# Performance work log

Measured on AMD Instinct MI355X. Metric: run time of the kernel, lower is better.

The kernel has to match this reference:

```python
import jax, jax.numpy as jnp
import numpy as np

N_NODES = 25000
N_EDGES = 400000
FEAT = 128
HID = 64
HEADS = 4
NUM_CLASSES = 2
NUM_GRAPHS = 64


def setup_inputs() -> dict:
    key = jax.random.key(0)
    ks = jax.random.split(key, 16)
    x = jax.random.normal(ks[0], (N_NODES, FEAT), dtype=jnp.float32)
    edge_index = jax.random.randint(ks[1], (2, N_EDGES), 0, N_NODES, dtype=jnp.int32)
    batch = jnp.sort(jax.random.randint(ks[2], (N_NODES,), 0, NUM_GRAPHS, dtype=jnp.int32))
    s = 1.0 / np.sqrt(FEAT)
    sh = 1.0 / np.sqrt(HID)
    shc = 1.0 / np.sqrt(HID * HEADS)
    return {
        "x": x,
        "edge_index": edge_index,
        "batch": batch,
        # conv1: GraphConv(FEAT -> HID): lin_rel (bias) on aggregated neighbors + lin_root (no bias)
        "W1_rel": jax.random.uniform(ks[3], (FEAT, HID), jnp.float32, -s, s),
        "b1": jnp.zeros((HID,), jnp.float32),
        "W1_root": jax.random.uniform(ks[4], (FEAT, HID), jnp.float32, -s, s),
        # conv3: GATConv(HID -> HID, heads=HEADS), concat output [N, HEADS*HID]
        "Wg": jax.random.uniform(ks[5], (HID, HEADS * HID), jnp.float32, -sh, sh),
        "att_src": jax.random.uniform(ks[6], (HEADS, HID), jnp.float32, -sh, sh),
        "att_dst": jax.random.uniform(ks[7], (HEADS, HID), jnp.float32, -sh, sh),
        "bg": jnp.zeros((HEADS * HID,), jnp.float32),
        # conv5: GraphConv(HEADS*HID -> HID)
        "W5_rel": jax.random.uniform(ks[8], (HEADS * HID, HID), jnp.float32, -shc, shc),
        "b5": jnp.zeros((HID,), jnp.float32),
        "W5_root": jax.random.uniform(ks[9], (HEADS * HID, HID), jnp.float32, -shc, shc),
        # fc head
        "W_fc1": jax.random.uniform(ks[10], (HID, HID), jnp.float32, -sh, sh),
        "b_fc1": jnp.zeros((HID,), jnp.float32),
        "W_fc2": jax.random.uniform(ks[11], (HID, NUM_CLASSES), jnp.float32, -sh, sh),
        "b_fc2": jnp.zeros((NUM_CLASSES,), jnp.float32),
    }


def _graph_conv(h, src, dst, W_rel, b, W_root):
    # PyG GraphConv (aggr='add'): out_i = W_rel @ sum_{j->i} h_j + b + W_root @ h_i
    agg = jax.ops.segment_sum(h[src], dst, num_segments=N_NODES)
    return agg @ W_rel + b + h @ W_root


def _gat_conv(h, src, dst, Wg, att_src, att_dst, bg):
    # GATConv with default add_self_loops=True; eval mode (no attn dropout)
    n = h.shape[0]
    loop = jnp.arange(n, dtype=src.dtype)
    si = jnp.concatenate([src, loop])
    di = jnp.concatenate([dst, loop])
    xl = (h @ Wg).reshape(n, HEADS, HID)              # [N, H, C]
    a_s = jnp.sum(xl * att_src, axis=-1)              # [N, H]
    a_d = jnp.sum(xl * att_dst, axis=-1)              # [N, H]
    e = jax.nn.leaky_relu(a_s[si] + a_d[di], 0.2)     # [E', H]
    m = jax.ops.segment_max(e, di, num_segments=n)
    p = jnp.exp(e - m[di])
    denom = jax.ops.segment_sum(p, di, num_segments=n)
    alpha = p / denom[di]                             # segment softmax over incoming edges
    out = jax.ops.segment_sum(alpha[:, :, None] * xl[si], di, num_segments=n)
    return out.reshape(n, HEADS * HID) + bg


def reference(x, edge_index, batch, W1_rel, b1, W1_root, Wg, att_src, att_dst, bg,
              W5_rel, b5, W5_root, W_fc1, b_fc1, W_fc2, b_fc2):
    src, dst = edge_index[0], edge_index[1]
    h = jax.nn.relu(_graph_conv(x, src, dst, W1_rel, b1, W1_root))
    h = jax.nn.relu(_gat_conv(h, src, dst, Wg, att_src, att_dst, bg))
    h = jax.nn.relu(_graph_conv(h, src, dst, W5_rel, b5, W5_root))
    g = jax.ops.segment_sum(h, batch, num_segments=NUM_GRAPHS)   # global_add_pool
    g = jax.nn.relu(g @ W_fc1 + b_fc1)
    return jax.nn.sigmoid(g @ W_fc2 + b_fc2)
```

## Files before the change

### kernel.cpp

```cpp
#include <hip/hip_runtime.h>
#include <math.h>

#define N_NODES 25000
#define N_EDGES 400000
#define FEAT 128
#define HID 64
#define HEADS 4
#define HH 256
#define NUM_GRAPHS 64
#define BUCKET 96

typedef unsigned short ushort_t;
typedef unsigned int uint_t;
typedef __attribute__((ext_vector_type(8))) short short8;
typedef __attribute__((ext_vector_type(4))) float f32x4;

__device__ __forceinline__ float lrelu(float x){ return x > 0.f ? x : 0.2f*x; }

__device__ __forceinline__ ushort_t f2bf(float f){
  uint_t u = __float_as_uint(f);
  return (ushort_t)((u + 0x7fffu + ((u >> 16) & 1u)) >> 16);
}
#define BF_LO(u) __uint_as_float((u) << 16)
#define BF_HI(u) __uint_as_float((u) & 0xffff0000u)

__global__ __launch_bounds__(256) void k_pack(
    const float* __restrict__ W1_rel, const float* __restrict__ W1_root,
    const float* __restrict__ W5_rel, const float* __restrict__ W5_root,
    const float* __restrict__ Wg,
    ushort_t* __restrict__ wc1b, ushort_t* __restrict__ wc5b,
    ushort_t* __restrict__ wgb)
{
  const int e = blockIdx.x*256 + threadIdx.x;
  {
    int j=e&7, lane=(e>>3)&63, kc=(e>>9)&3, nt=e>>11;
    int k = kc*32 + (lane>>4)*8 + j, n = nt*16 + (lane&15);
    float v = (n < 64) ? W1_rel[k*64 + n] : W1_root[k*64 + n - 64];
    wc1b[e] = f2bf(v);
  }
  {
    int j=e&7, lane=(e>>3)&63, kt=(e>>9)&1, nt=e>>10;
    int k = kt*32 + (lane>>4)*8 + j, n = nt*16 + (lane&15);
    wgb[e] = f2bf(Wg[k*HH + n]);
  }
  #pragma unroll
  for (int e5 = e; e5 < 32768; e5 += 16384){
    int j=e5&7, lane=(e5>>3)&63, kc=(e5>>9)&7, nt=e5>>12;
    int k = kc*32 + (lane>>4)*8 + j, n = nt*16 + (lane&15);
    float v = (n < 64) ? W5_rel[k*64 + n] : W5_root[k*64 + n - 64];
    wc5b[e5] = f2bf(v);
  }
}

__global__ __launch_bounds__(256) void conv1_mfma(
    const float* __restrict__ X, const ushort_t* __restrict__ wc1b,
    const float* __restrict__ bias,
    ushort_t* __restrict__ out_rel_b, float* __restrict__ out_root)
{
  const int wid  = __builtin_amdgcn_readfirstlane(threadIdx.x >> 6);
  const int lane = threadIdx.x & 63;
  const int quad = lane >> 4, col = lane & 15;
  const int nb = blockIdx.x*64 + wid*16;
  if (nb >= N_NODES) return;
  const int row = min(nb + col, N_NODES-1);
  const float* __restrict__ xr = X + (size_t)row*FEAT + quad*8;
  short8 a[4];
  #pragma unroll
  for (int kc = 0; kc < 4; kc++){
    #pragma unroll
    for (int j = 0; j < 8; j++)
      ((ushort_t*)&a[kc])[j] = f2bf(xr[kc*32 + j]);
  }
  #pragma unroll
  for (int nt = 0; nt < 8; nt++){
    f32x4 d = {0.f,0.f,0.f,0.f};
    #pragma unroll
    for (int kc = 0; kc < 4; kc++){
      short8 b = *(const short8*)(wc1b + ((size_t)(nt*4+kc)*64 + lane)*8);
      d = __builtin_amdgcn_mfma_f32_16x16x32_bf16(a[kc], b, d, 0, 0, 0);
    }
    if (nt < 4){
      #pragma unroll
      for (int r = 0; r < 4; r++){
        const int node = nb + quad*4 + r;
        if (node < N_NODES)
          out_rel_b[(size_t)node*HID + nt*16 + col] = f2bf(d[r]);
      }
    } else {
      const float bv = bias[(nt-4)*16 + col];
      #pragma unroll
      for (int r = 0; r < 4; r++){
        const int node = nb + quad*4 + r;
        if (node < N_NODES)
          out_root[(size_t)node*HID + (nt-4)*16 + col] = d[r] + bv;
      }
    }
  }
}

__global__ __launch_bounds__(256) void conv5_mfma(
    const ushort_t* __restrict__ h2b, const ushort_t* __restrict__ wc5b,
    const float* __restrict__ bias,
    ushort_t* __restrict__ out_rel_b, float* __restrict__ out_root)
{
  const int wid  = __builtin_amdgcn_readfirstlane(threadIdx.x >> 6);
  const int lane = threadIdx.x & 63;
  const int quad = lane >> 4, col = lane & 15;
  const int nb = blockIdx.x*64 + wid*16;
  if (nb >= N_NODES) return;
  const ushort_t* __restrict__ arow = h2b + (size_t)(nb + col)*HH + quad*8;
  short8 a[8];
  #pragma unroll
  for (int kc = 0; kc < 8; kc++)
    a[kc] = *(const short8*)(arow + kc*32);
  #pragma unroll
  for (int nt = 0; nt < 8; nt++){
    f32x4 d = {0.f,0.f,0.f,0.f};
    #pragma unroll
    for (int kc = 0; kc < 8; kc++){
      short8 b = *(const short8*)(wc5b + ((size_t)(nt*8+kc)*64 + lane)*8);
      d = __builtin_amdgcn_mfma_f32_16x16x32_bf16(a[kc], b, d, 0, 0, 0);
    }
    if (nt < 4){
      #pragma unroll
      for (int r = 0; r < 4; r++){
        const int node = nb + quad*4 + r;
        if (node < N_NODES)
          out_rel_b[(size_t)node*HID + nt*16 + col] = f2bf(d[r]);
      }
    } else {
      const float bv = bias[(nt-4)*16 + col];
      #pragma unroll
      for (int r = 0; r < 4; r++){
        const int node = nb + quad*4 + r;
        if (node < N_NODES)
          out_root[(size_t)node*HID + (nt-4)*16 + col] = d[r] + bv;
      }
    }
  }
}

__global__ __launch_bounds__(256) void k3_mfma(
    const ushort_t* __restrict__ h1b, const ushort_t* __restrict__ wgb,
    const float* __restrict__ att_src, const float* __restrict__ att_dst,
    ushort_t* __restrict__ xlb, float* __restrict__ a_s, float* __restrict__ a_d)
{
  const int wid  = __builtin_amdgcn_readfirstlane(threadIdx.x >> 6);
  const int lane = threadIdx.x & 63;
  const int quad = lane >> 4, col = lane & 15;
  const int nb = blockIdx.x*64 + wid*16;
  const ushort_t* arow = h1b + (size_t)(nb + col)*HID + quad*8;
  short8 a0 = *(const short8*)(arow);
  short8 a1 = *(const short8*)(arow + 32);
  float as_acc[4] = {0,0,0,0}, ad_acc[4] = {0,0,0,0};
  #pragma unroll
  for (int nt = 0; nt < 16; nt++){
    short8 b0 = *(const short8*)(wgb + ((size_t)(nt*2+0)*64 + lane)*8);
    short8 b1 = *(const short8*)(wgb + ((size_t)(nt*2+1)*64 + lane)*8);
    f32x4 d = {0.f, 0.f, 0.f, 0.f};
    d = __builtin_amdgcn_mfma_f32_16x16x32_bf16(a0, b0, d, 0, 0, 0);
    d = __builtin_amdgcn_mfma_f32_16x16x32_bf16(a1, b1, d, 0, 0, 0);
    const int h = nt >> 2;
    const float asv = att_src[h*HID + (nt & 3)*16 + col];
    const float adv = att_dst[h*HID + (nt & 3)*16 + col];
    #pragma unroll
    for (int r = 0; r < 4; r++){
      const int node = nb + quad*4 + r;
      if (node < N_NODES)
        xlb[(size_t)node*HH + nt*16 + col] = f2bf(d[r]);
      as_acc[r] += d[r]*asv;
      ad_acc[r] += d[r]*adv;
    }
    if ((nt & 3) == 3){
      #pragma unroll
      for (int r = 0; r < 4; r++){
        float s1 = as_acc[r], s2 = ad_acc[r];
        #pragma unroll
        for (int off = 1; off < 16; off <<= 1){
          s1 += __shfl_xor(s1, off, 64);
          s2 += __shfl_xor(s2, off, 64);
        }
        const int node = nb + quad*4 + r;
        if (col == 0 && node < N_NODES){
          a_s[node*HEADS + h] = s1;
          a_d[node*HEADS + h] = s2;
        }
        as_acc[r] = 0.f; ad_acc[r] = 0.f;
      }
    }
  }
}

__global__ __launch_bounds__(256) void k_fill(const int* __restrict__ src,
                                              const int* __restrict__ dst,
                                              int* __restrict__ cnt,
                                              int* __restrict__ slot)
{
  int e = blockIdx.x*256 + threadIdx.x;
  if (e >= N_EDGES) return;
  int d = dst[e];
  int pos = atomicAdd(&cnt[d], 1);
  if (pos < BUCKET) slot[(size_t)d*BUCKET + pos] = src[e];
}

template<bool BF16OUT>
__global__ __launch_bounds__(256) void k_aggb(
    const int* __restrict__ cnt, const int* __restrict__ slot,
    const ushort_t* __restrict__ featb, const float* __restrict__ root,
    float* __restrict__ outf, ushort_t* __restrict__ outb)
{
  const int node = blockIdx.x*4 + (threadIdx.x >> 6);
  const int lane = threadIdx.x & 63;
  const int* __restrict__ sl = slot + (size_t)node*BUCKET;
  const int deg = min(cnt[node], BUCKET);
  float acc = root[(size_t)node*HID + lane];
  int e = 0;
  for (; e + 4 <= deg; e += 4){
    int sA = sl[e],   sB = sl[e+1];
    int sC = sl[e+2], sD = sl[e+3];
    float xA = BF_LO((uint_t)featb[(size_t)sA*HID + lane]);
    float xB = BF_LO((uint_t)featb[(size_t)sB*HID + lane]);
    float xC = BF_LO((uint_t)featb[(size_t)sC*HID + lane]);
    float xD = BF_LO((uint_t)featb[(size_t)sD*HID + lane]);
    acc += xA; acc += xB; acc += xC; acc += xD;
  }
  for (; e < deg; e++){
    int s = sl[e];
    acc += BF_LO((uint_t)featb[(size_t)s*HID + lane]);
  }
  const float v = fmaxf(acc, 0.f);
  if (BF16OUT) outb[(size_t)node*HID + lane] = f2bf(v);
  else         outf[(size_t)node*HID + lane] = v;
}

__global__ __launch_bounds__(256) void k_gat_node(
    const int* __restrict__ cnt, const int* __restrict__ slot,
    const uint2* __restrict__ xl2,
    const float* __restrict__ a_s, const float* __restrict__ a_d,
    const float* __restrict__ bg, ushort_t* __restrict__ h2b)
{
  const int node = blockIdx.x*4 + (threadIdx.x >> 6);
  const int lane = threadIdx.x & 63;
  const int h  = lane >> 4;
  const int el = lane & 15;
  const int* __restrict__ sl = slot + (size_t)node*BUCKET;
  const int deg = min(cnt[node], BUCKET);
  const float adh = a_d[node*HEADS + h];
  float acc0=0, acc1=0, acc2=0, acc3=0;
  float dsum = 0.f;
  for (int base = 0; base < deg; base += 16){
    float pme = 0.f; int sme = node;
    const int e = base + el;
    if (e < deg){
      sme = sl[e];
      pme = __expf(lrelu(a_s[sme*HEADS + h] + adh));
    }
    dsum += pme;
    const int nsub = min(16, deg - base);
    int e4 = 0;
    for (; e4 + 2 <= nsub; e4 += 2){
      const int b0 = (lane & 48) + e4;
      const float pA = __shfl(pme, b0, 64);
      const int   sA = __shfl(sme, b0, 64);
      const float pB = __shfl(pme, b0 + 1, 64);
      const int   sB = __shfl(sme, b0 + 1, 64);
      uint2 rA = xl2[(size_t)sA*64 + lane];
      uint2 rB = xl2[(size_t)sB*64 + lane];
      acc0 += pA*BF_LO(rA.x); acc1 += pA*BF_HI(rA.x);
      acc2 += pA*BF_LO(rA.y); acc3 += pA*BF_HI(rA.y);
      acc0 += pB*BF_LO(rB.x); acc1 += pB*BF_HI(rB.x);
      acc2 += pB*BF_LO(rB.y); acc3 += pB*BF_HI(rB.y);
    }
    if (e4 < nsub){
      const int b0 = (lane & 48) + e4;
      const float pA = __shfl(pme, b0, 64);
      const int   sA = __shfl(sme, b0, 64);
      uint2 rA = xl2[(size_t)sA*64 + lane];
      acc0 += pA*BF_LO(rA.x); acc1 += pA*BF_HI(rA.x);
      acc2 += pA*BF_LO(rA.y); acc3 += pA*BF_HI(rA.y);
    }
  }
  #pragma unroll
  for (int off = 1; off < 16; off <<= 1) dsum += __shfl_xor(dsum, off, 64);
  const float pself = __expf(lrelu(a_s[node*HEADS + h] + adh));
  const float inv = 1.f / (dsum + pself);
  uint2 r = xl2[(size_t)node*64 + lane];
  acc0 += pself*BF_LO(r.x); acc1 += pself*BF_HI(r.x);
  acc2 += pself*BF_LO(r.y); acc3 += pself*BF_HI(r.y);
  const int col0 = lane*4;
  const float ox = fmaxf(acc0*inv + bg[col0+0], 0.f);
  const float oy = fmaxf(acc1*inv + bg[col0+1], 0.f);
  const float oz = fmaxf(acc2*inv + bg[col0+2], 0.f);
  const float ow = fmaxf(acc3*inv + bg[col0+3], 0.f);
  uint2 o;
  o.x = (uint_t)f2bf(ox) | ((uint_t)f2bf(oy) << 16);
  o.y = (uint_t)f2bf(oz) | ((uint_t)f2bf(ow) << 16);
  ((uint2*)(h2b + (size_t)node*HH))[lane] = o;
}

__global__ __launch_bounds__(256) void k_pool(
    const float* __restrict__ h3, const int* __restrict__ batch,
    float* __restrict__ g)
{
  const int w = blockIdx.x*4 + (threadIdx.x >> 6);
  const int j = threadIdx.x & 63;
  int n0 = w*64;
  if (n0 >= N_NODES) return;
  int n1 = min(n0+64, N_NODES);
  float acc = 0.f;
  int cur = batch[n0];
  for (int n = n0; n < n1; n++){
    int b = batch[n];
    if (b != cur){ atomicAdd(&g[cur*HID + j], acc); acc = 0.f; cur = b; }
    acc += h3[n*HID + j];
  }
  atomicAdd(&g[cur*HID + j], acc);
}

__global__ __launch_bounds__(256) void k_head(
    const float* __restrict__ g, const float* __restrict__ W1,
    const float* __restrict__ b1, const float* __restrict__ W2,
    const float* __restrict__ b2, float* __restrict__ out)
{
  __shared__ float gs[NUM_GRAPHS*HID];
  __shared__ float hh[NUM_GRAPHS*HID];
  for (int i = threadIdx.x; i < NUM_GRAPHS*HID; i += 256) gs[i] = g[i];
  __syncthreads();
  for (int t = threadIdx.x; t < NUM_GRAPHS*HID; t += 256){
    int b = t >> 6, j = t & 63;
    float acc = b1[j];
    for (int k = 0; k < HID; k++) acc += gs[b*HID+k]*W1[k*HID+j];
    hh[t] = fmaxf(acc, 0.f);
  }
  __syncthreads();
  for (int t = threadIdx.x; t < NUM_GRAPHS*2; t += 256){
    int b = t >> 1, c = t & 1;
    float acc = b2[c];
    for (int k = 0; k < HID; k++) acc += hh[b*HID+k]*W2[k*2+c];
    out[t] = 1.f / (1.f + __expf(-acc));
  }
}

extern "C" void kernel_launch(void* const* d_in, const int* in_sizes, int n_in,
                              void* d_out, int out_size, void* d_ws, size_t ws_size,
                              hipStream_t stream)
{
  const float* x       = (const float*)d_in[0];
  const int*   ei      = (const int*)d_in[1];
  const int*   batch   = (const int*)d_in[2];
  const float* W1_rel  = (const float*)d_in[3];
  const float* b1      = (const float*)d_in[4];
  const float* W1_root = (const float*)d_in[5];
  const float* Wg      = (const float*)d_in[6];
  const float* att_src = (const float*)d_in[7];
  const float* att_dst = (const float*)d_in[8];
  const float* bg      = (const float*)d_in[9];
  const float* W5_rel  = (const float*)d_in[10];
  const float* b5      = (const float*)d_in[11];
  const float* W5_root = (const float*)d_in[12];
  const float* W_fc1   = (const float*)d_in[13];
  const float* b_fc1   = (const float*)d_in[14];
  const float* W_fc2   = (const float*)d_in[15];
  const float* b_fc2   = (const float*)d_in[16];
  const int* src = ei;
  const int* dst = ei + N_EDGES;

  float* ws    = (float*)d_ws;
  ushort_t* xr_b = (ushort_t*)ws;
  float* hB    = ws +   800000;
  ushort_t* h1b = (ushort_t*)(ws + 2400000);
  ushort_t* xlb = (ushort_t*)(ws + 3200768);
  float* a_s   = ws +  6400768;
  float* a_d   = ws +  6500768;
  ushort_t* h2b = (ushort_t*)(ws + 6600768);
  float* g     = ws +  9803840;
  int*   cnt   = (int*)(ws + 9807936);
  ushort_t* wc1b = (ushort_t*)(ws + 9833600);
  ushort_t* wc5b = (ushort_t*)(ws + 9841792);
  ushort_t* wgb  = (ushort_t*)(ws + 9858176);
  int*   slot  = (int*)(ws + 9870000);
  float* out   = (float*)d_out;

  hipMemsetAsync(g, 0, (4096 + N_NODES)*sizeof(float), stream);
  k_fill<<<(N_EDGES+255)/256,256,0,stream>>>(src, dst, cnt, slot);
  k_pack<<<64,256,0,stream>>>(W1_rel, W1_root, W5_rel, W5_root, Wg,
                              wc1b, wc5b, wgb);

  conv1_mfma<<<(N_NODES+63)/64,256,0,stream>>>(x, wc1b, b1, xr_b, hB);
  k_aggb<true><<<N_NODES/4,256,0,stream>>>(cnt, slot, xr_b, hB, nullptr, h1b);

  k3_mfma<<<(N_NODES+63)/64,256,0,stream>>>(h1b, wgb, att_src, att_dst,
                                            xlb, a_s, a_d);
  k_gat_node<<<N_NODES/4,256,0,stream>>>(cnt, slot,
      (const uint2*)xlb, a_s, a_d, bg, h2b);

  conv5_mfma<<<(N_NODES+63)/64,256,0,stream>>>(h2b, wc5b, b5, xr_b, hB);
  k_aggb<false><<<N_NODES/4,256,0,stream>>>(cnt, slot, xr_b, hB, hB, nullptr);

  k_pool<<<(N_NODES/256)+1,256,0,stream>>>(hB, batch, g);
  k_head<<<1,256,0,stream>>>(g, W_fc1, b_fc1, W_fc2, b_fc2, out);
}
```

Measured before the change: 255.1 us.

## Split GAT features into head-major planes and parallelize GAT aggregation per head

Stores the GAT projected features, attention scores and GAT output in head-major planes, so each head's 64-wide slice is a contiguous 128-byte row. The GAT aggregation kernel now runs one block per (node group, head), with four edges gathered concurrently per wave and a cross-group shuffle reduction at the end. conv5 reads its input from the head-major planes. The weight-packing kernel is also folded into the edge-bucketing kernel to save a launch. This raises gather parallelism and spreads head work across four times as many blocks, at the cost of redundant neighbor-index and degree reads per head, extra shuffles, and a guard that skips zero-probability lanes.

```diff
diff --git a/kernel.cpp b/kernel.cpp
--- a/kernel.cpp
+++ b/kernel.cpp
@@ -9,6 +9,8 @@
 #define HH 256
 #define NUM_GRAPHS 64
 #define BUCKET 96
+#define HS 1601536
+#define NPH 25600
 
 typedef unsigned short ushort_t;
 typedef unsigned int uint_t;
@@ -24,7 +26,9 @@
 #define BF_LO(u) __uint_as_float((u) << 16)
 #define BF_HI(u) __uint_as_float((u) & 0xffff0000u)
 
-__global__ __launch_bounds__(256) void k_pack(
+__global__ __launch_bounds__(256) void k_fill(
+    const int* __restrict__ src, const int* __restrict__ dst,
+    int* __restrict__ cnt, int* __restrict__ slot,
     const float* __restrict__ W1_rel, const float* __restrict__ W1_root,
     const float* __restrict__ W5_rel, const float* __restrict__ W5_root,
     const float* __restrict__ Wg,
@@ -32,23 +36,30 @@
     ushort_t* __restrict__ wgb)
 {
   const int e = blockIdx.x*256 + threadIdx.x;
-  {
-    int j=e&7, lane=(e>>3)&63, kc=(e>>9)&3, nt=e>>11;
-    int k = kc*32 + (lane>>4)*8 + j, n = nt*16 + (lane&15);
-    float v = (n < 64) ? W1_rel[k*64 + n] : W1_root[k*64 + n - 64];
-    wc1b[e] = f2bf(v);
-  }
-  {
-    int j=e&7, lane=(e>>3)&63, kt=(e>>9)&1, nt=e>>10;
-    int k = kt*32 + (lane>>4)*8 + j, n = nt*16 + (lane&15);
-    wgb[e] = f2bf(Wg[k*HH + n]);
-  }
-  #pragma unroll
-  for (int e5 = e; e5 < 32768; e5 += 16384){
-    int j=e5&7, lane=(e5>>3)&63, kc=(e5>>9)&7, nt=e5>>12;
-    int k = kc*32 + (lane>>4)*8 + j, n = nt*16 + (lane&15);
-    float v = (n < 64) ? W5_rel[k*64 + n] : W5_root[k*64 + n - 64];
-    wc5b[e5] = f2bf(v);
+  if (blockIdx.x < 64){
+    {
+      int j=e&7, lane=(e>>3)&63, kc=(e>>9)&3, nt=e>>11;
+      int k = kc*32 + (lane>>4)*8 + j, n = nt*16 + (lane&15);
+      float v = (n < 64) ? W1_rel[k*64 + n] : W1_root[k*64 + n - 64];
+      wc1b[e] = f2bf(v);
+    }
+    {
+      int j=e&7, lane=(e>>3)&63, kt=(e>>9)&1, nt=e>>10;
+      int k = kt*32 + (lane>>4)*8 + j, n = nt*16 + (lane&15);
+      wgb[e] = f2bf(Wg[k*HH + n]);
+    }
+    #pragma unroll
+    for (int e5 = e; e5 < 32768; e5 += 16384){
+      int j=e5&7, lane=(e5>>3)&63, kc=(e5>>9)&7, nt=e5>>12;
+      int k = kc*32 + (lane>>4)*8 + j, n = nt*16 + (lane&15);
+      float v = (n < 64) ? W5_rel[k*64 + n] : W5_root[k*64 + n - 64];
+      wc5b[e5] = f2bf(v);
+    }
+  }
+  if (e < N_EDGES){
+    int d = dst[e];
+    int pos = atomicAdd(&cnt[d], 1);
+    if (pos < BUCKET) slot[(size_t)d*BUCKET + pos] = src[e];
   }
 }
 
@@ -99,7 +110,7 @@
 }
 
 __global__ __launch_bounds__(256) void conv5_mfma(
-    const ushort_t* __restrict__ h2b, const ushort_t* __restrict__ wc5b,
+    const ushort_t* __restrict__ h2b_hm, const ushort_t* __restrict__ wc5b,
     const float* __restrict__ bias,
     ushort_t* __restrict__ out_rel_b, float* __restrict__ out_root)
 {
@@ -108,11 +119,14 @@
   const int quad = lane >> 4, col = lane & 15;
   const int nb = blockIdx.x*64 + wid*16;
   if (nb >= N_NODES) return;
-  const ushort_t* __restrict__ arow = h2b + (size_t)(nb + col)*HH + quad*8;
+  const int row = nb + col;
   short8 a[8];
   #pragma unroll
-  for (int kc = 0; kc < 8; kc++)
-    a[kc] = *(const short8*)(arow + kc*32);
+  for (int kc = 0; kc < 8; kc++){
+    const int k0 = kc*32 + quad*8;
+    a[kc] = *(const short8*)(h2b_hm + (size_t)(k0>>6)*HS
+                             + (size_t)row*HID + (k0&63));
+  }
   #pragma unroll
   for (int nt = 0; nt < 8; nt++){
     f32x4 d = {0.f,0.f,0.f,0.f};
@@ -143,7 +157,8 @@
 __global__ __launch_bounds__(256) void k3_mfma(
     const ushort_t* __restrict__ h1b, const ushort_t* __restrict__ wgb,
     const float* __restrict__ att_src, const float* __restrict__ att_dst,
-    ushort_t* __restrict__ xlb, float* __restrict__ a_s, float* __restrict__ a_d)
+    ushort_t* __restrict__ xlb_hm, float* __restrict__ a_s_hm,
+    float* __restrict__ a_d_hm)
 {
   const int wid  = __builtin_amdgcn_readfirstlane(threadIdx.x >> 6);
   const int lane = threadIdx.x & 63;
@@ -167,7 +182,7 @@
     for (int r = 0; r < 4; r++){
       const int node = nb + quad*4 + r;
       if (node < N_NODES)
-        xlb[(size_t)node*HH + nt*16 + col] = f2bf(d[r]);
+        xlb_hm[(size_t)h*HS + (size_t)node*HID + (nt&3)*16 + col] = f2bf(d[r]);
       as_acc[r] += d[r]*asv;
       ad_acc[r] += d[r]*adv;
     }
@@ -182,25 +197,13 @@
         }
         const int node = nb + quad*4 + r;
         if (col == 0 && node < N_NODES){
-          a_s[node*HEADS + h] = s1;
-          a_d[node*HEADS + h] = s2;
+          a_s_hm[h*NPH + node] = s1;
+          a_d_hm[h*NPH + node] = s2;
         }
         as_acc[r] = 0.f; ad_acc[r] = 0.f;
       }
     }
   }
-}
-
-__global__ __launch_bounds__(256) void k_fill(const int* __restrict__ src,
-                                              const int* __restrict__ dst,
-                                              int* __restrict__ cnt,
-                                              int* __restrict__ slot)
-{
-  int e = blockIdx.x*256 + threadIdx.x;
-  if (e >= N_EDGES) return;
-  int d = dst[e];
-  int pos = atomicAdd(&cnt[d], 1);
-  if (pos < BUCKET) slot[(size_t)d*BUCKET + pos] = src[e];
 }
 
 template<bool BF16OUT>
@@ -235,67 +238,63 @@
 
 __global__ __launch_bounds__(256) void k_gat_node(
     const int* __restrict__ cnt, const int* __restrict__ slot,
-    const uint2* __restrict__ xl2,
-    const float* __restrict__ a_s, const float* __restrict__ a_d,
-    const float* __restrict__ bg, ushort_t* __restrict__ h2b)
-{
-  const int node = blockIdx.x*4 + (threadIdx.x >> 6);
+    const ushort_t* __restrict__ xlb_hm, const float* __restrict__ a_s_hm,
+    const float* __restrict__ a_d_hm, const float* __restrict__ bg,
+    ushort_t* __restrict__ h2b_hm)
+{
+  const int head = blockIdx.x & 3;
+  const int node = (blockIdx.x >> 2)*4 + (threadIdx.x >> 6);
   const int lane = threadIdx.x & 63;
-  const int h  = lane >> 4;
-  const int el = lane & 15;
+  const int eg = lane >> 4, cl = lane & 15;
   const int* __restrict__ sl = slot + (size_t)node*BUCKET;
   const int deg = min(cnt[node], BUCKET);
-  const float adh = a_d[node*HEADS + h];
+  const ushort_t* __restrict__ xlh = xlb_hm + (size_t)head*HS;
+  const float* __restrict__ ash = a_s_hm + head*NPH;
+  const float adh = a_d_hm[head*NPH + node];
   float acc0=0, acc1=0, acc2=0, acc3=0;
   float dsum = 0.f;
   for (int base = 0; base < deg; base += 16){
     float pme = 0.f; int sme = node;
-    const int e = base + el;
+    const int e = base + cl;
     if (e < deg){
       sme = sl[e];
-      pme = __expf(lrelu(a_s[sme*HEADS + h] + adh));
-    }
-    dsum += pme;
-    const int nsub = min(16, deg - base);
-    int e4 = 0;
-    for (; e4 + 2 <= nsub; e4 += 2){
-      const int b0 = (lane & 48) + e4;
-      const float pA = __shfl(pme, b0, 64);
-      const int   sA = __shfl(sme, b0, 64);
-      const float pB = __shfl(pme, b0 + 1, 64);
-      const int   sB = __shfl(sme, b0 + 1, 64);
-      uint2 rA = xl2[(size_t)sA*64 + lane];
-      uint2 rB = xl2[(size_t)sB*64 + lane];
-      acc0 += pA*BF_LO(rA.x); acc1 += pA*BF_HI(rA.x);
-      acc2 += pA*BF_LO(rA.y); acc3 += pA*BF_HI(rA.y);
-      acc0 += pB*BF_LO(rB.x); acc1 += pB*BF_HI(rB.x);
-      acc2 += pB*BF_LO(rB.y); acc3 += pB*BF_HI(rB.y);
-    }
-    if (e4 < nsub){
-      const int b0 = (lane & 48) + e4;
-      const float pA = __shfl(pme, b0, 64);
-      const int   sA = __shfl(sme, b0, 64);
-      uint2 rA = xl2[(size_t)sA*64 + lane];
-      acc0 += pA*BF_LO(rA.x); acc1 += pA*BF_HI(rA.x);
-      acc2 += pA*BF_LO(rA.y); acc3 += pA*BF_HI(rA.y);
-    }
-  }
+      pme = __expf(lrelu(ash[sme] + adh));
+    }
+    if (eg == 0) dsum += pme;
+    #pragma unroll
+    for (int s = 0; s < 4; s++){
+      const int e2 = s*4 + eg;
+      const float p = __shfl(pme, e2, 64);
+      if (p > 0.f){
+        const int sidx = __shfl(sme, e2, 64);
+        uint2 r = ((const uint2*)(xlh + (size_t)sidx*HID))[cl];
+        acc0 += p*BF_LO(r.x); acc1 += p*BF_HI(r.x);
+        acc2 += p*BF_LO(r.y); acc3 += p*BF_HI(r.y);
+      }
+    }
+  }
+  acc0 += __shfl_xor(acc0,16,64); acc0 += __shfl_xor(acc0,32,64);
+  acc1 += __shfl_xor(acc1,16,64); acc1 += __shfl_xor(acc1,32,64);
+  acc2 += __shfl_xor(acc2,16,64); acc2 += __shfl_xor(acc2,32,64);
+  acc3 += __shfl_xor(acc3,16,64); acc3 += __shfl_xor(acc3,32,64);
   #pragma unroll
   for (int off = 1; off < 16; off <<= 1) dsum += __shfl_xor(dsum, off, 64);
-  const float pself = __expf(lrelu(a_s[node*HEADS + h] + adh));
+  const float pself = __expf(lrelu(ash[node] + adh));
   const float inv = 1.f / (dsum + pself);
-  uint2 r = xl2[(size_t)node*64 + lane];
+  uint2 r = ((const uint2*)(xlh + (size_t)node*HID))[cl];
   acc0 += pself*BF_LO(r.x); acc1 += pself*BF_HI(r.x);
   acc2 += pself*BF_LO(r.y); acc3 += pself*BF_HI(r.y);
-  const int col0 = lane*4;
-  const float ox = fmaxf(acc0*inv + bg[col0+0], 0.f);
-  const float oy = fmaxf(acc1*inv + bg[col0+1], 0.f);
-  const float oz = fmaxf(acc2*inv + bg[col0+2], 0.f);
-  const float ow = fmaxf(acc3*inv + bg[col0+3], 0.f);
-  uint2 o;
-  o.x = (uint_t)f2bf(ox) | ((uint_t)f2bf(oy) << 16);
-  o.y = (uint_t)f2bf(oz) | ((uint_t)f2bf(ow) << 16);
-  ((uint2*)(h2b + (size_t)node*HH))[lane] = o;
+  if (eg == 0){
+    const int col0 = head*HID + cl*4;
+    const float ox = fmaxf(acc0*inv + bg[col0+0], 0.f);
+    const float oy = fmaxf(acc1*inv + bg[col0+1], 0.f);
+    const float oz = fmaxf(acc2*inv + bg[col0+2], 0.f);
+    const float ow = fmaxf(acc3*inv + bg[col0+3], 0.f);
+    uint2 o;
+    o.x = (uint_t)f2bf(ox) | ((uint_t)f2bf(oy) << 16);
+    o.y = (uint_t)f2bf(oz) | ((uint_t)f2bf(ow) << 16);
+    ((uint2*)(h2b_hm + (size_t)head*HS + (size_t)node*HID))[cl] = o;
+  }
 }
 
 __global__ __launch_bounds__(256) void k_pool(
@@ -366,35 +365,34 @@
   const int* dst = ei + N_EDGES;
 
   float* ws    = (float*)d_ws;
-  ushort_t* xr_b = (ushort_t*)ws;
-  float* hB    = ws +   800000;
-  ushort_t* h1b = (ushort_t*)(ws + 2400000);
-  ushort_t* xlb = (ushort_t*)(ws + 3200768);
-  float* a_s   = ws +  6400768;
-  float* a_d   = ws +  6500768;
-  ushort_t* h2b = (ushort_t*)(ws + 6600768);
-  float* g     = ws +  9803840;
-  int*   cnt   = (int*)(ws + 9807936);
-  ushort_t* wc1b = (ushort_t*)(ws + 9833600);
-  ushort_t* wc5b = (ushort_t*)(ws + 9841792);
-  ushort_t* wgb  = (ushort_t*)(ws + 9858176);
-  int*   slot  = (int*)(ws + 9870000);
-  float* out   = (float*)d_out;
+  ushort_t* xr_b   = (ushort_t*)ws;
+  float*    hB     = ws +  800800;
+  ushort_t* h1b    = (ushort_t*)(ws + 2402400);
+  ushort_t* xlb_hm = (ushort_t*)(ws + 3203200);
+  float*    a_s_hm = ws + 6406304;
+  float*    a_d_hm = ws + 6508704;
+  ushort_t* h2b_hm = (ushort_t*)(ws + 6611104);
+  float*    g      = ws + 9814200;
+  int*      cnt    = (int*)(ws + 9818296);
+  ushort_t* wc1b   = (ushort_t*)(ws + 9843296);
+  ushort_t* wc5b   = (ushort_t*)(ws + 9851488);
+  ushort_t* wgb    = (ushort_t*)(ws + 9867872);
+  int*      slot   = (int*)(ws + 9876064);
+  float*    out    = (float*)d_out;
 
   hipMemsetAsync(g, 0, (4096 + N_NODES)*sizeof(float), stream);
-  k_fill<<<(N_EDGES+255)/256,256,0,stream>>>(src, dst, cnt, slot);
-  k_pack<<<64,256,0,stream>>>(W1_rel, W1_root, W5_rel, W5_root, Wg,
-                              wc1b, wc5b, wgb);
+  k_fill<<<(N_EDGES+255)/256,256,0,stream>>>(src, dst, cnt, slot,
+      W1_rel, W1_root, W5_rel, W5_root, Wg, wc1b, wc5b, wgb);
 
   conv1_mfma<<<(N_NODES+63)/64,256,0,stream>>>(x, wc1b, b1, xr_b, hB);
   k_aggb<true><<<N_NODES/4,256,0,stream>>>(cnt, slot, xr_b, hB, nullptr, h1b);
 
   k3_mfma<<<(N_NODES+63)/64,256,0,stream>>>(h1b, wgb, att_src, att_dst,
-                                            xlb, a_s, a_d);
-  k_gat_node<<<N_NODES/4,256,0,stream>>>(cnt, slot,
-      (const uint2*)xlb, a_s, a_d, bg, h2b);
-
-  conv5_mfma<<<(N_NODES+63)/64,256,0,stream>>>(h2b, wc5b, b5, xr_b, hB);
+                                            xlb_hm, a_s_hm, a_d_hm);
+  k_gat_node<<<N_NODES/4*HEADS,256,0,stream>>>(cnt, slot,
+      xlb_hm, a_s_hm, a_d_hm, bg, h2b_hm);
+
+  conv5_mfma<<<(N_NODES+63)/64,256,0,stream>>>(h2b_hm, wc5b, b5, xr_b, hB);
   k_aggb<false><<<N_NODES/4,256,0,stream>>>(cnt, slot, xr_b, hB, hB, nullptr);
 
   k_pool<<<(N_NODES/256)+1,256,0,stream>>>(hB, batch, g);
```

After: 278.3 us. 1.09x slower.
